# Optimization experiments

Measured on AMD Instinct MI355X. Metric: run time of the kernel, lower is better.

## Reference

```python
import jax, jax.numpy as jnp
import numpy as np
from jax import lax


def setup_inputs() -> dict:
    key = jax.random.key(0)
    kx, kf = jax.random.split(key)
    x = jax.random.normal(kx, (64, 3, 224, 224), dtype=jnp.float32)
    filters = jax.random.normal(kf, (16, 3, 3, 3), dtype=jnp.float32)
    return {"x": x, "filters": filters}


def reference(x, filters):
    # Faithful math of the naive per-position matmul conv: a standard VALID
    # cross-correlation (no bias), stride=1, padding=0. Filters are OIHW.
    out = lax.conv_general_dilated(
        x, filters,
        window_strides=(1, 1),
        padding='VALID',
        dimension_numbers=('NCHW', 'OIHW', 'NCHW'),
    )
    return out  # [B, out_channels, H-k+1, W-k+1]
```

## Files before the change

### kernel.cpp

```cpp
#include <hip/hip_runtime.h>


namespace {
constexpr int B  = 64, C = 3, H = 224, W = 224;
constexpr int OC = 16, KS = 3, OH = 222, OW = 222;
constexpr int NW4   = 56;
constexpr int TOTAL = B * OH * NW4;
constexpr int BLOCK = 256;
typedef float f32x2 __attribute__((ext_vector_type(2)));
}

__global__ __launch_bounds__(BLOCK, 4) void conv3x3_kernel(
    const float* __restrict__ x, const float* __restrict__ flt,
    float* __restrict__ out) {
  const int tid = blockIdx.x * BLOCK + threadIdx.x;
  const int g  = tid % NW4;
  const int t1 = tid / NW4;
  const int oh = t1 % OH;
  const int b  = t1 / OH;
  const int w0 = g * 4;
  const bool tail = (g == NW4 - 1);
  const int  wb   = tail ? w0 : w0 + 4;

  float c8[C][KS][8];
  const float* xb = x + (size_t)b * (C * H * W);
#pragma unroll
  for (int c = 0; c < C; ++c) {
#pragma unroll
    for (int r = 0; r < KS; ++r) {
      const float* row = xb + (c * H + oh + r) * W;
      const float4 a  = *reinterpret_cast<const float4*>(row + w0);
      const float4 bb = *reinterpret_cast<const float4*>(row + wb);
      c8[c][r][0] = a.x;  c8[c][r][1] = a.y;  c8[c][r][2] = a.z;  c8[c][r][3] = a.w;
      c8[c][r][4] = bb.x; c8[c][r][5] = bb.y; c8[c][r][6] = bb.z; c8[c][r][7] = bb.w;
    }
  }

  float* outp = out + (size_t)(b * OC) * (OH * OW) + (size_t)oh * OW + w0;
#pragma unroll 1
  for (int oc = 0; oc < OC; ++oc) {
    float fv[27];
#pragma unroll
    for (int k = 0; k < 27; ++k) fv[k] = flt[oc * 27 + k];

    float a0 = 0.f, a1 = 0.f, a2 = 0.f, a3 = 0.f;
#pragma unroll
    for (int c = 0; c < C; ++c)
#pragma unroll
      for (int r = 0; r < KS; ++r)
#pragma unroll
        for (int kw = 0; kw < KS; ++kw) {
          const float wv = fv[c * 9 + r * 3 + kw];
          a0 = fmaf(wv, c8[c][r][kw + 0], a0);
          a1 = fmaf(wv, c8[c][r][kw + 1], a1);
          a2 = fmaf(wv, c8[c][r][kw + 2], a2);
          a3 = fmaf(wv, c8[c][r][kw + 3], a3);
        }

    float* op = outp + (size_t)oc * (OH * OW);
    if (!tail) {
      f32x2 v01; v01.x = a0; v01.y = a1;
      f32x2 v23; v23.x = a2; v23.y = a3;
      __builtin_nontemporal_store(v01, reinterpret_cast<f32x2*>(op));
      __builtin_nontemporal_store(v23, reinterpret_cast<f32x2*>(op) + 1);
    } else {
      __builtin_nontemporal_store(a0, op + 0);
      __builtin_nontemporal_store(a1, op + 1);
    }
  }
}

extern "C" void kernel_launch(void* const* d_in, const int* in_sizes, int n_in,
                              void* d_out, int out_size, void* d_ws, size_t ws_size,
                              hipStream_t stream) {
  const float* x = (const float*)d_in[0];
  const float* f = (const float*)d_in[1];
  float* o       = (float*)d_out;
  const int grid = TOTAL / BLOCK;
  conv3x3_kernel<<<grid, BLOCK, 0, stream>>>(x, f, o);
}
```

Baseline: 243.3 us.

## Map one wavefront per output row and align float4 stores for odd rows

Reorganizes the thread mapping so each 64-lane wavefront handles one output row of a 4-row block, with 56 active lanes per row. Because OW=222, odd rows are not 16-byte aligned, so the column windows for odd rows are shifted by two and the loaded data is permuted in registers. This lets every lane issue a single 16-byte nontemporal store instead of two 8-byte stores, with special-case lanes at the row edges. The cost is 8 idle lanes per wave, extra select instructions on odd rows, and idle warps in the last row block.

```diff
diff --git a/kernel.cpp b/kernel.cpp
--- a/kernel.cpp
+++ b/kernel.cpp
@@ -4,39 +4,59 @@
 namespace {
 constexpr int B  = 64, C = 3, H = 224, W = 224;
 constexpr int OC = 16, KS = 3, OH = 222, OW = 222;
-constexpr int NW4   = 56;
-constexpr int TOTAL = B * OH * NW4;
 constexpr int BLOCK = 256;
+constexpr int RPB   = 4;
+constexpr int NOG   = (OH + RPB - 1) / RPB;
+constexpr int GRID  = B * NOG;
 typedef float f32x2 __attribute__((ext_vector_type(2)));
+typedef float f32x4 __attribute__((ext_vector_type(4)));
 }
 
 __global__ __launch_bounds__(BLOCK, 4) void conv3x3_kernel(
     const float* __restrict__ x, const float* __restrict__ flt,
     float* __restrict__ out) {
-  const int tid = blockIdx.x * BLOCK + threadIdx.x;
-  const int g  = tid % NW4;
-  const int t1 = tid / NW4;
-  const int oh = t1 % OH;
-  const int b  = t1 / OH;
-  const int w0 = g * 4;
-  const bool tail = (g == NW4 - 1);
-  const int  wb   = tail ? w0 : w0 + 4;
+  const int wid  = threadIdx.x >> 6;
+  const int lane = threadIdx.x & 63;
+  const int bb   = blockIdx.x / NOG;
+  const int og   = blockIdx.x % NOG;
+  const int oh   = og * RPB + wid;
+  if (oh >= OH) return;
 
-  float c8[C][KS][8];
-  const float* xb = x + (size_t)b * (C * H * W);
+  const bool odd = (oh & 1) != 0;
+  const int  s      = lane < 56 ? lane : 55;
+  const bool active = lane < 56;
+  const bool l0  = odd && (s == 0);
+  const bool e55 = !odd && (s == 55);
+  const int ow0 = odd ? 4 * s - 2 : 4 * s;
+  const int la = odd ? (s == 0 ? 0 : 4 * s - 4) : (s == 55 ? 220 : 4 * s);
+  const int lb = e55 ? la : la + 4;
+
+  float c8[C * KS][8];
+  const float* xb = x + (size_t)bb * (C * H * W);
 #pragma unroll
   for (int c = 0; c < C; ++c) {
 #pragma unroll
     for (int r = 0; r < KS; ++r) {
       const float* row = xb + (c * H + oh + r) * W;
-      const float4 a  = *reinterpret_cast<const float4*>(row + w0);
-      const float4 bb = *reinterpret_cast<const float4*>(row + wb);
-      c8[c][r][0] = a.x;  c8[c][r][1] = a.y;  c8[c][r][2] = a.z;  c8[c][r][3] = a.w;
-      c8[c][r][4] = bb.x; c8[c][r][5] = bb.y; c8[c][r][6] = bb.z; c8[c][r][7] = bb.w;
+      const f32x4 a  = *reinterpret_cast<const f32x4*>(row + la);
+      const f32x4 bv = *reinterpret_cast<const f32x4*>(row + lb);
+      float* w = c8[c * KS + r];
+      w[0] = a.x;  w[1] = a.y;  w[2] = a.z;  w[3] = a.w;
+      w[4] = bv.x; w[5] = bv.y; w[6] = bv.z; w[7] = bv.w;
+      if (odd) {
+        const float t0 = w[0], t1 = w[1], t2 = w[2], t3 = w[3];
+        w[0] = l0 ? t0 : w[2];
+        w[1] = l0 ? t1 : w[3];
+        w[2] = l0 ? t0 : w[4];
+        w[3] = l0 ? t1 : w[5];
+        w[4] = l0 ? t2 : w[6];
+        w[5] = l0 ? t3 : w[7];
+      }
     }
   }
 
-  float* outp = out + (size_t)(b * OC) * (OH * OW) + (size_t)oh * OW + w0;
+  const size_t ocs = (size_t)OH * OW;
+  float* op0 = out + (size_t)bb * OC * ocs + (size_t)oh * OW;
 #pragma unroll 1
   for (int oc = 0; oc < OC; ++oc) {
     float fv[27];
@@ -47,25 +67,30 @@
 #pragma unroll
     for (int c = 0; c < C; ++c)
 #pragma unroll
-      for (int r = 0; r < KS; ++r)
+      for (int r = 0; r < KS; ++r) {
+        const float* w = c8[c * KS + r];
 #pragma unroll
         for (int kw = 0; kw < KS; ++kw) {
-          const float wv = fv[c * 9 + r * 3 + kw];
-          a0 = fmaf(wv, c8[c][r][kw + 0], a0);
-          a1 = fmaf(wv, c8[c][r][kw + 1], a1);
-          a2 = fmaf(wv, c8[c][r][kw + 2], a2);
-          a3 = fmaf(wv, c8[c][r][kw + 3], a3);
+          const float f = fv[c * 9 + r * 3 + kw];
+          a0 = fmaf(f, w[kw + 0], a0);
+          a1 = fmaf(f, w[kw + 1], a1);
+          a2 = fmaf(f, w[kw + 2], a2);
+          a3 = fmaf(f, w[kw + 3], a3);
         }
+      }
 
-    float* op = outp + (size_t)oc * (OH * OW);
-    if (!tail) {
-      f32x2 v01; v01.x = a0; v01.y = a1;
-      f32x2 v23; v23.x = a2; v23.y = a3;
-      __builtin_nontemporal_store(v01, reinterpret_cast<f32x2*>(op));
-      __builtin_nontemporal_store(v23, reinterpret_cast<f32x2*>(op) + 1);
-    } else {
-      __builtin_nontemporal_store(a0, op + 0);
-      __builtin_nontemporal_store(a1, op + 1);
+    if (active) {
+      float* op = op0 + (size_t)oc * ocs;
+      if (l0) {
+        f32x2 v; v.x = a2; v.y = a3;
+        __builtin_nontemporal_store(v, reinterpret_cast<f32x2*>(op));
+      } else if (e55) {
+        f32x2 v; v.x = a0; v.y = a1;
+        __builtin_nontemporal_store(v, reinterpret_cast<f32x2*>(op + 220));
+      } else {
+        f32x4 v; v.x = a0; v.y = a1; v.z = a2; v.w = a3;
+        __builtin_nontemporal_store(v, reinterpret_cast<f32x4*>(op + ow0));
+      }
     }
   }
 }
@@ -76,6 +101,5 @@
   const float* x = (const float*)d_in[0];
   const float* f = (const float*)d_in[1];
   float* o       = (float*)d_out;
-  const int grid = TOTAL / BLOCK;
-  conv3x3_kernel<<<grid, BLOCK, 0, stream>>>(x, f, o);
+  conv3x3_kernel<<<GRID, BLOCK, 0, stream>>>(x, f, o);
 }
```

Result: slower. 251.5 us (+3.4%).
